# Performance work log

Measured on AMD Instinct MI355X. Metric: run time of the kernel, lower is better.

## Reference

```python
import jax, jax.numpy as jnp
import numpy as np

S = 2048      # sequence length
E = 2048      # n_embd
H = 16        # n_head
D = E // H    # head_dim = 128
EPS = 1e-5


def _layer_norm(x, w):
    # eqx.nn.LayerNorm, use_bias=False: (x - mean) / sqrt(var + eps) * w
    mu = jnp.mean(x, axis=-1, keepdims=True)
    var = jnp.mean(jnp.square(x - mu), axis=-1, keepdims=True)
    return (x - mu) * jax.lax.rsqrt(var + EPS) * w


def setup_inputs() -> dict:
    key = jax.random.key(0)
    ks = jax.random.split(key, 7)
    x = jax.random.normal(ks[0], (S, E), dtype=jnp.float32)
    # equinox Linear weights are (out_features, in_features); y = W @ x
    w_attn = jax.random.normal(ks[1], (3 * E, E), dtype=jnp.float32) * 0.02
    w_proj_attn = jax.random.normal(ks[2], (E, E), dtype=jnp.float32) * 0.02
    w_fc = jax.random.normal(ks[3], (4 * E, E), dtype=jnp.float32) * 0.02
    w_proj_ffn = jax.random.normal(ks[4], (E, 4 * E), dtype=jnp.float32) * 0.02
    ln1_w = jnp.ones((E,), dtype=jnp.float32)
    ln2_w = jnp.ones((E,), dtype=jnp.float32)
    return {"x": x, "ln1_w": ln1_w, "ln2_w": ln2_w, "w_attn": w_attn,
            "w_proj_attn": w_proj_attn, "w_fc": w_fc, "w_proj_ffn": w_proj_ffn}


def reference(x, ln1_w, ln2_w, w_attn, w_proj_attn, w_fc, w_proj_ffn):
    # --- LN1 + fused QKV projection ---
    h = _layer_norm(x, ln1_w)                       # [S, E]
    qkv = h @ w_attn.T                              # [S, 3E]
    q, k, v = jnp.split(qkv, 3, axis=-1)
    q = q.reshape(S, H, D)
    k = k.reshape(S, H, D)
    v = v.reshape(S, H, D)
    # --- naive causal attention with materialized [H, S, T] scores ---
    scale = 1.0 / jnp.sqrt(jnp.float32(D))
    causal_bias = (jnp.arange(S)[:, None] < jnp.arange(S)[None, :]) * (-10000.0)
    scores = jnp.einsum('shd,thd->hst', q, k) * scale + causal_bias  # [H,S,T]
    probs = jax.nn.softmax(scores, axis=-1)
    attn = jnp.einsum('hst,thd->shd', probs, v).reshape(S, E)
    x = x + attn @ w_proj_attn.T
    # --- LN2 + GELU MLP ---
    h2 = _layer_norm(x, ln2_w)                      # [S, E]
    f = jax.nn.gelu(h2 @ w_fc.T) @ w_proj_ffn.T    # [S,4E] -> [S,E]
    return x + f
```

## Files before the change

kernel.cpp:

```cpp
#include <hip/hip_runtime.h>
#include <hip/hip_bf16.h>

#define S_LEN 2048
#define EMB   2048
#define NH    16
#define HD    128

typedef __bf16 bf16x8 __attribute__((ext_vector_type(8)));
typedef __bf16 bf16x4 __attribute__((ext_vector_type(4)));
typedef float  f32x4  __attribute__((ext_vector_type(4)));
typedef short  s16x4  __attribute__((ext_vector_type(4)));

__device__ __forceinline__ void async_copy16(void* lds, const void* g) {
  __builtin_amdgcn_global_load_lds((__attribute__((address_space(1))) void*)(void*)g,
                                   (__attribute__((address_space(3))) void*)lds, 16, 0, 0);
}

__device__ __forceinline__ unsigned lds_addr(const void* p) {
  return (unsigned)(uintptr_t)(const __attribute__((address_space(3))) char*)p;
}

__device__ __forceinline__ s16x4 tr16(unsigned addr) {
  s16x4 d;
  asm volatile("ds_read_b64_tr_b16 %0, %1" : "=v"(d) : "v"(addr));
  return d;
}

__device__ __forceinline__ float gelu_tanh(float x) {
  float x3 = x * x * x;
  float t  = 0.7978845608028654f * (x + 0.044715f * x3);
  float th = 1.0f - 2.0f / (__expf(2.0f * t) + 1.0f);
  return 0.5f * x * (1.0f + th);
}

__global__ __launch_bounds__(256) void cast_kernel(const float* __restrict__ in,
                                                   __bf16* __restrict__ out, int n) {
  int i = (blockIdx.x * 256 + threadIdx.x) * 4;
  if (i >= n) return;
  float4 v = *(const float4*)(in + i);
  bf16x4 o;
  o[0] = (__bf16)v.x; o[1] = (__bf16)v.y; o[2] = (__bf16)v.z; o[3] = (__bf16)v.w;
  *(bf16x4*)(out + i) = o;
}

__global__ __launch_bounds__(256) void ln_kernel(const float* __restrict__ x,
                                                 const float* __restrict__ w,
                                                 __bf16* __restrict__ out) {
  int row = blockIdx.x;
  int t = threadIdx.x;
  const float* xr = x + (size_t)row * EMB;
  float4 a = *(const float4*)(xr + t * 8);
  float4 b = *(const float4*)(xr + t * 8 + 4);
  float s  = a.x + a.y + a.z + a.w + b.x + b.y + b.z + b.w;
  float sq = a.x*a.x + a.y*a.y + a.z*a.z + a.w*a.w + b.x*b.x + b.y*b.y + b.z*b.z + b.w*b.w;
  #pragma unroll
  for (int o = 32; o > 0; o >>= 1) { s += __shfl_xor(s, o); sq += __shfl_xor(sq, o); }
  __shared__ float red[8];
  if ((t & 63) == 0) { red[t >> 6] = s; red[(t >> 6) + 4] = sq; }
  __syncthreads();
  s  = red[0] + red[1] + red[2] + red[3];
  sq = red[4] + red[5] + red[6] + red[7];
  float mu  = s * (1.0f / EMB);
  float var = sq * (1.0f / EMB) - mu * mu;
  float rs  = rsqrtf(var + 1e-5f);
  float4 w1 = *(const float4*)(w + t * 8);
  float4 w2 = *(const float4*)(w + t * 8 + 4);
  bf16x8 ov;
  ov[0] = (__bf16)((a.x - mu) * rs * w1.x);
  ov[1] = (__bf16)((a.y - mu) * rs * w1.y);
  ov[2] = (__bf16)((a.z - mu) * rs * w1.z);
  ov[3] = (__bf16)((a.w - mu) * rs * w1.w);
  ov[4] = (__bf16)((b.x - mu) * rs * w2.x);
  ov[5] = (__bf16)((b.y - mu) * rs * w2.y);
  ov[6] = (__bf16)((b.z - mu) * rs * w2.z);
  ov[7] = (__bf16)((b.w - mu) * rs * w2.w);
  *(bf16x8*)(out + (size_t)row * EMB + t * 8) = ov;
}

__global__ __launch_bounds__(256) void ln_fuse_kernel(const float* __restrict__ x,
                                                      const __bf16* __restrict__ part,
                                                      const float* __restrict__ w,
                                                      __bf16* __restrict__ hout,
                                                      float* __restrict__ resout) {
  int row = blockIdx.x;
  int t = threadIdx.x;
  const size_t base = (size_t)row * EMB + t * 8;
  float r[8];
  {
    float4 a = *(const float4*)(x + base);
    float4 b = *(const float4*)(x + base + 4);
    r[0] = a.x; r[1] = a.y; r[2] = a.z; r[3] = a.w;
    r[4] = b.x; r[5] = b.y; r[6] = b.z; r[7] = b.w;
    #pragma unroll
    for (int z = 0; z < 4; z++) {
      bf16x8 p = *(const bf16x8*)(part + (size_t)z * S_LEN * EMB + base);
      #pragma unroll
      for (int k = 0; k < 8; k++) r[k] += (float)p[k];
    }
  }
  float s = 0.f, sq = 0.f;
  #pragma unroll
  for (int k = 0; k < 8; k++) { s += r[k]; sq += r[k] * r[k]; }
  #pragma unroll
  for (int o = 32; o > 0; o >>= 1) { s += __shfl_xor(s, o); sq += __shfl_xor(sq, o); }
  __shared__ float red[8];
  if ((t & 63) == 0) { red[t >> 6] = s; red[(t >> 6) + 4] = sq; }
  __syncthreads();
  s  = red[0] + red[1] + red[2] + red[3];
  sq = red[4] + red[5] + red[6] + red[7];
  float mu  = s * (1.0f / EMB);
  float var = sq * (1.0f / EMB) - mu * mu;
  float rs  = rsqrtf(var + 1e-5f);
  float4 w1 = *(const float4*)(w + t * 8);
  float4 w2 = *(const float4*)(w + t * 8 + 4);
  float wv[8] = {w1.x, w1.y, w1.z, w1.w, w2.x, w2.y, w2.z, w2.w};
  bf16x8 ov;
  #pragma unroll
  for (int k = 0; k < 8; k++) ov[k] = (__bf16)((r[k] - mu) * rs * wv[k]);
  *(bf16x8*)(hout + base) = ov;
  float4 o1 = make_float4(r[0], r[1], r[2], r[3]);
  float4 o2 = make_float4(r[4], r[5], r[6], r[7]);
  *(float4*)(resout + base) = o1;
  *(float4*)(resout + base + 4) = o2;
}

__global__ __launch_bounds__(256) void add4_kernel(float* __restrict__ out,
                                                   const __bf16* __restrict__ part) {
  size_t i = ((size_t)blockIdx.x * 256 + threadIdx.x) * 4;
  float4 o = *(const float4*)(out + i);
  #pragma unroll
  for (int z = 0; z < 4; z++) {
    bf16x4 p = *(const bf16x4*)(part + (size_t)z * S_LEN * EMB + i);
    o.x += (float)p[0]; o.y += (float)p[1]; o.z += (float)p[2]; o.w += (float)p[3];
  }
  *(float4*)(out + i) = o;
}

#define MFMA16(AV, BV, MG)                                                                   \
  _Pragma("unroll")                                                                          \
  for (int m = 0; m < 4; m++)                                                                \
    _Pragma("unroll")                                                                        \
    for (int n = 0; n < 4; n++)                                                              \
      acc[(MG) * 4 + m][n] =                                                                 \
          __builtin_amdgcn_mfma_f32_16x16x32_bf16(AV[m], BV[n], acc[(MG) * 4 + m][n], 0, 0, 0);

#define PHASE_TOP()                                                                          \
  __builtin_amdgcn_s_barrier();                                                              \
  __builtin_amdgcn_s_setprio(1);

#define PHASE_BOT()                                                                          \
  __builtin_amdgcn_s_setprio(0);                                                             \
  __builtin_amdgcn_s_barrier();

template <int EPI>
__global__ __launch_bounds__(512, 2) void gemm256(const __bf16* __restrict__ A,
                                                  const __bf16* __restrict__ B,
                                                  void* __restrict__ Cv,
                                                  int M, int N, int K, int Ksl,
                                                  int NN, int NSPLIT) {
  __shared__ __bf16 As[2 * 2 * 256 * 32];
  __shared__ __bf16 Bs[2 * 2 * 256 * 32];

  const int t = threadIdx.x, w = t >> 6, l = t & 63;
  const int fr = l & 15, g = l >> 4;
  const int wr = w >> 2, wc = w & 3;

  const int nwg = gridDim.x;
  const int wg = (blockIdx.x & 7) * (nwg >> 3) + (blockIdx.x >> 3);
  const int z = wg % NSPLIT;
  const int tile = wg / NSPLIT;
  const int my = tile / NN, nx = tile - my * NN;
  const int m0 = my * 256, n0 = nx * 256;
  const int kb = z * Ksl;
  const int NT = Ksl >> 6;

  const int srow = t >> 2;
  const int schunk = (t & 3) ^ ((t >> 3) & 3);
  const __bf16* Abase = A + (size_t)(m0 + srow) * K + kb + schunk * 8;
  const __bf16* Bbase = B + (size_t)(n0 + srow) * K + kb + schunk * 8;
  const size_t K128 = (size_t)128 * K;
  __bf16* AsT = &As[t * 8];
  __bf16* BsT = &Bs[t * 8];

  auto stage = [&](const __bf16* base, __bf16* dstT, int kt, int kh) {
    const __bf16* src = base + kt * 64 + kh * 32;
    __bf16* dst = dstT + ((kt & 1) * 2 + kh) * 8192;
    async_copy16(dst, src);
    async_copy16(dst + 4096, src + K128);
  };

  const int gran = (g ^ ((fr >> 1) & 3)) << 3;
  auto rdA = [&](bf16x8* dst, int kt, int kh, int mg) {
    const int ub = ((kt & 1) * 2 + kh) * 256;
    #pragma unroll
    for (int m = 0; m < 4; m++) {
      int row = wr * 128 + (mg * 4 + m) * 16 + fr;
      dst[m] = *(const bf16x8*)&As[(ub + row) * 32 + gran];
    }
  };
  auto rdB = [&](bf16x8* dst, int kt, int kh) {
    const int ub = ((kt & 1) * 2 + kh) * 256;
    #pragma unroll
    for (int n = 0; n < 4; n++) {
      int row = wc * 64 + n * 16 + fr;
      dst[n] = *(const bf16x8*)&Bs[(ub + row) * 32 + gran];
    }
  };

  f32x4 acc[8][4] = {};
  bf16x8 av[4], bX[4], bY[4];

  stage(Abase, AsT, 0, 0); stage(Bbase, BsT, 0, 0);
  stage(Abase, AsT, 0, 1); stage(Bbase, BsT, 0, 1);
  if (NT > 1) { stage(Abase, AsT, 1, 0); stage(Bbase, BsT, 1, 0); }
  asm volatile("s_waitcnt vmcnt(4)" ::: "memory");
  __builtin_amdgcn_s_barrier();

  for (int kt = 0; kt < NT; ++kt) {
    const bool s1 = (kt + 1 < NT), s2 = (kt + 2 < NT);
    rdB(bX, kt, 0);
    rdA(av, kt, 0, 0);
    if (s1) stage(Abase, AsT, kt + 1, 1);
    PHASE_TOP();
    MFMA16(av, bX, 0);
    PHASE_BOT();
    rdA(av, kt, 0, 1);
    if (s1) stage(Bbase, BsT, kt + 1, 1);
    PHASE_TOP();
    MFMA16(av, bX, 1);
    __builtin_amdgcn_s_setprio(0);
    if (s1) { asm volatile("s_waitcnt vmcnt(4)" ::: "memory"); }
    else    { asm volatile("s_waitcnt vmcnt(0)" ::: "memory"); }
    __builtin_amdgcn_s_barrier();
    rdB(bY, kt, 1);
    rdA(av, kt, 1, 0);
    if (s2) stage(Abase, AsT, kt + 2, 0);
    PHASE_TOP();
    MFMA16(av, bY, 0);
    PHASE_BOT();
    rdA(av, kt, 1, 1);
    if (s2) stage(Bbase, BsT, kt + 2, 0);
    PHASE_TOP();
    MFMA16(av, bY, 1);
    PHASE_BOT();
  }

  const size_t zoff = (size_t)z * M * N;
  #pragma unroll
  for (int m = 0; m < 8; m++)
    #pragma unroll
    for (int n = 0; n < 4; n++)
      #pragma unroll
      for (int j = 0; j < 4; j++) {
        int orow = m0 + wr * 128 + m * 16 + g * 4 + j;
        int ocol = n0 + wc * 64 + n * 16 + fr;
        size_t idx = (size_t)orow * N + ocol;
        float v = acc[m][n][j];
        if (EPI == 0) {
          ((__bf16*)Cv)[idx] = (__bf16)v;
        } else if (EPI == 2) {
          ((__bf16*)Cv)[idx] = (__bf16)gelu_tanh(v);
        } else {
          ((__bf16*)Cv)[zoff + idx] = (__bf16)v;
        }
      }
}

__global__ __launch_bounds__(512, 2) void attn_kernel(const __bf16* __restrict__ qkv,
                                                      __bf16* __restrict__ out) {
  __shared__ __bf16 Kt[2][64 * 128];
  __shared__ __bf16 Vt[2][64 * 128];
  __shared__ __bf16 Pb[8][16 * 64];

  const int bid = blockIdx.x;
  const int h = bid & 15;
  const int pi = bid >> 4;
  const int qbA = pi, qbB = 31 - pi;

  const int t = threadIdx.x, w = t >> 6, l = t & 63;
  const int g = l >> 4, fr = l & 15;
  const int fkb = g * 8;
  const int myqb = (w < 4) ? qbA : qbB;
  const int q0 = myqb * 64 + (w & 3) * 16;
  const float scale = 0.08838834764831845f;

  const int kchunk = fr ^ ((w * 4 + g) & 7);
  const int vkey = (l >> 1) & 3;
  const int vd0  = (l >> 3) * 16 + (l & 1) * 8;

  const size_t row3E = (size_t)(3 * EMB);
  const __bf16* Kg = qkv + EMB + h * HD;
  const __bf16* Vg = qkv + 2 * EMB + h * HD;

  bf16x8 qf[4];
  #pragma unroll
  for (int kc = 0; kc < 4; kc++)
    qf[kc] = *(const bf16x8*)&qkv[(size_t)(q0 + fr) * row3E + h * HD + kc * 32 + fkb];

  f32x4 o[8] = {};
  float mrun[4] = {-1e30f, -1e30f, -1e30f, -1e30f};
  float lsum[4] = {0.f, 0.f, 0.f, 0.f};

  const unsigned vtrb[2] = { lds_addr(&Vt[0][0]) + g * 2048 + fr * 8,
                             lds_addr(&Vt[1][0]) + g * 2048 + fr * 8 };

  auto stage = [&](int buf, int it) {
    const int t0 = it * 64;
    #pragma unroll
    for (int r = 0; r < 2; r++) {
      async_copy16(&Kt[buf][(r * 8 + w) * 512],
                   Kg + (size_t)(t0 + (r * 8 + w) * 4 + g) * row3E + kchunk * 8);
      async_copy16(&Vt[buf][(r * 8 + w) * 512],
                   Vg + (size_t)(t0 + (r * 8 + w) * 4 + vkey) * row3E + vd0);
    }
  };

  const int nt = qbB + 1;
  stage(0, 0);
  int cur = 0;

  for (int it = 0; it < nt; it++) {
    __syncthreads();
    if (it + 1 < nt) stage(cur ^ 1, it + 1);

    if (it <= myqb) {
      const int t0 = it * 64;
      f32x4 s[4] = {};
      __builtin_amdgcn_s_setprio(1);
      #pragma unroll
      for (int n = 0; n < 4; n++)
        #pragma unroll
        for (int kc = 0; kc < 4; kc++) {
          bf16x8 kf = *(const bf16x8*)&Kt[cur][(n * 16 + fr) * 128 +
                                              (((kc * 4 + g) ^ (fr & 7)) << 3)];
          s[n] = __builtin_amdgcn_mfma_f32_16x16x32_bf16(qf[kc], kf, s[n], 0, 0, 0);
        }
      __builtin_amdgcn_s_setprio(0);
      #pragma unroll
      for (int n = 0; n < 4; n++)
        #pragma unroll
        for (int j = 0; j < 4; j++) {
          int tcol = t0 + n * 16 + fr;
          int qrow = q0 + g * 4 + j;
          float v = s[n][j] * scale;
          s[n][j] = (tcol > qrow) ? -1e30f : v;
        }
      float pm[4];
      #pragma unroll
      for (int j = 0; j < 4; j++) {
        pm[j] = fmaxf(fmaxf(s[0][j], s[1][j]), fmaxf(s[2][j], s[3][j]));
        #pragma unroll
        for (int off = 1; off < 16; off <<= 1) pm[j] = fmaxf(pm[j], __shfl_xor(pm[j], off));
      }
      float factor[4];
      #pragma unroll
      for (int j = 0; j < 4; j++) {
        float mn = fmaxf(mrun[j], pm[j]);
        factor[j] = __expf(mrun[j] - mn);
        mrun[j] = mn;
      }
      float rs[4] = {0.f, 0.f, 0.f, 0.f};
      #pragma unroll
      for (int n = 0; n < 4; n++)
        #pragma unroll
        for (int j = 0; j < 4; j++) {
          float p = __expf(s[n][j] - mrun[j]);
          s[n][j] = p;
          rs[j] += p;
        }
      #pragma unroll
      for (int j = 0; j < 4; j++) {
        #pragma unroll
        for (int off = 1; off < 16; off <<= 1) rs[j] += __shfl_xor(rs[j], off);
        lsum[j] = lsum[j] * factor[j] + rs[j];
      }
      #pragma unroll
      for (int b = 0; b < 8; b++)
        #pragma unroll
        for (int j = 0; j < 4; j++) o[b][j] *= factor[j];

      #pragma unroll
      for (int n = 0; n < 4; n++)
        #pragma unroll
        for (int j = 0; j < 4; j++) {
          int q   = g * 4 + j;
          int key = n * 16 + fr;
          int cs  = (key >> 3) ^ (q & 7);
          Pb[w][q * 64 + cs * 8 + (key & 7)] = (__bf16)s[n][j];
        }

      bf16x8 pf[2];
      #pragma unroll
      for (int kc = 0; kc < 2; kc++)
        pf[kc] = *(const bf16x8*)&Pb[w][fr * 64 + (((kc * 4 + g) ^ (fr & 7)) << 3)];

      const unsigned vtr = vtrb[cur];
      __builtin_amdgcn_s_setprio(1);
      #pragma unroll
      for (int b = 0; b < 8; b++) {
        s16x4 t00 = tr16(vtr + b * 128);
        s16x4 t01 = tr16(vtr + b * 128 + 1024);
        s16x4 t10 = tr16(vtr + b * 128 + 8192);
        s16x4 t11 = tr16(vtr + b * 128 + 8192 + 1024);
        asm volatile("s_waitcnt lgkmcnt(0)");
        __builtin_amdgcn_sched_barrier(0);
        union { s16x4 hh[2]; bf16x8 v; } u0, u1;
        u0.hh[0] = t00; u0.hh[1] = t01;
        u1.hh[0] = t10; u1.hh[1] = t11;
        o[b] = __builtin_amdgcn_mfma_f32_16x16x32_bf16(pf[0], u0.v, o[b], 0, 0, 0);
        o[b] = __builtin_amdgcn_mfma_f32_16x16x32_bf16(pf[1], u1.v, o[b], 0, 0, 0);
      }
      __builtin_amdgcn_s_setprio(0);
    }
    cur ^= 1;
  }

  float rcp[4];
  #pragma unroll
  for (int j = 0; j < 4; j++) rcp[j] = 1.0f / lsum[j];
  #pragma unroll
  for (int b = 0; b < 8; b++)
    #pragma unroll
    for (int j = 0; j < 4; j++) {
      int qrow = q0 + g * 4 + j;
      out[(size_t)qrow * EMB + h * HD + b * 16 + fr] = (__bf16)(o[b][j] * rcp[j]);
    }
}

extern "C" void kernel_launch(void* const* d_in, const int* in_sizes, int n_in,
                              void* d_out, int out_size, void* d_ws, size_t ws_size,
                              hipStream_t stream) {
  const float* x     = (const float*)d_in[0];
  const float* ln1w  = (const float*)d_in[1];
  const float* ln2w  = (const float*)d_in[2];
  const float* wattn = (const float*)d_in[3];
  const float* wproja= (const float*)d_in[4];
  const float* wfc   = (const float*)d_in[5];
  const float* wprojf= (const float*)d_in[6];
  float* out = (float*)d_out;
  char* ws = (char*)d_ws;

  __bf16* wattn_b  = (__bf16*)(ws);
  __bf16* wproja_b = (__bf16*)(ws + 25165824);
  __bf16* wfc_b    = (__bf16*)(ws + 33554432);
  __bf16* wprojf_b = (__bf16*)(ws + 67108864);
  __bf16* h_b      = (__bf16*)(ws + 100663296);
  __bf16* qkv_b    = (__bf16*)(ws + 109051904);
  __bf16* attn_b   = (__bf16*)(ws + 134217728);
  __bf16* f1_b     = (__bf16*)(ws + 142606336);
  __bf16* p1_part  = f1_b;
  __bf16* p2_part  = qkv_b;

  cast_kernel<<<12288, 256, 0, stream>>>(wattn,  wattn_b,  12582912);
  cast_kernel<<<4096,  256, 0, stream>>>(wproja, wproja_b, 4194304);
  cast_kernel<<<16384, 256, 0, stream>>>(wfc,    wfc_b,    16777216);
  cast_kernel<<<16384, 256, 0, stream>>>(wprojf, wprojf_b, 16777216);

  ln_kernel<<<S_LEN, 256, 0, stream>>>(x, ln1w, h_b);
  gemm256<0><<<192, 512, 0, stream>>>(h_b, wattn_b, qkv_b, S_LEN, 3 * EMB, EMB, EMB, 24, 1);
  attn_kernel<<<dim3(256), 512, 0, stream>>>(qkv_b, attn_b);
  gemm256<5><<<256, 512, 0, stream>>>(attn_b, wproja_b, p1_part, S_LEN, EMB, EMB, EMB / 4, 8, 4);
  ln_fuse_kernel<<<S_LEN, 256, 0, stream>>>(x, p1_part, ln2w, h_b, out);
  gemm256<2><<<256, 512, 0, stream>>>(h_b, wfc_b, f1_b, S_LEN, 4 * EMB, EMB, EMB, 32, 1);
  gemm256<5><<<256, 512, 0, stream>>>(f1_b, wprojf_b, p2_part, S_LEN, EMB, 4 * EMB, 2048, 8, 4);
  add4_kernel<<<4096, 256, 0, stream>>>(out, p2_part);
}
```

Measured before the change: 403.7 us.

## Replace 256x256 GEMM with 128x256 tile, 3-stage K32 pipeline

Replaces the 256x256 GEMM tile, which double-buffered K=64 in two halves, with a 128x256 tile that uses a triple-buffered K=32 LDS pipeline and one barrier per iteration. The launch grids double and launch bounds raise occupancy to 4 blocks per CU, aiming to fill all CUs better and cut per-wave accumulator registers. The trade-off is lower arithmetic intensity per tile, more global traffic for B, and more barriers per unit of K work.

Result: slower. 418.1 us (+3.5%).

```diff
diff --git a/kernel.cpp b/kernel.cpp
--- a/kernel.cpp
+++ b/kernel.cpp
@@ -136,30 +136,14 @@
   *(float4*)(out + i) = o;
 }
 
-#define MFMA16(AV, BV, MG)                                                                   \
-  _Pragma("unroll")                                                                          \
-  for (int m = 0; m < 4; m++)                                                                \
-    _Pragma("unroll")                                                                        \
-    for (int n = 0; n < 4; n++)                                                              \
-      acc[(MG) * 4 + m][n] =                                                                 \
-          __builtin_amdgcn_mfma_f32_16x16x32_bf16(AV[m], BV[n], acc[(MG) * 4 + m][n], 0, 0, 0);
-
-#define PHASE_TOP()                                                                          \
-  __builtin_amdgcn_s_barrier();                                                              \
-  __builtin_amdgcn_s_setprio(1);
-
-#define PHASE_BOT()                                                                          \
-  __builtin_amdgcn_s_setprio(0);                                                             \
-  __builtin_amdgcn_s_barrier();
-
 template <int EPI>
-__global__ __launch_bounds__(512, 2) void gemm256(const __bf16* __restrict__ A,
+__global__ __launch_bounds__(512, 4) void gemm128(const __bf16* __restrict__ A,
                                                   const __bf16* __restrict__ B,
                                                   void* __restrict__ Cv,
                                                   int M, int N, int K, int Ksl,
                                                   int NN, int NSPLIT) {
-  __shared__ __bf16 As[2 * 2 * 256 * 32];
-  __shared__ __bf16 Bs[2 * 2 * 256 * 32];
+  __shared__ __bf16 As[3][128 * 32];
+  __shared__ __bf16 Bs[3][256 * 32];
 
   const int t = threadIdx.x, w = t >> 6, l = t & 63;
   const int fr = l & 15, g = l >> 4;
@@ -170,89 +154,66 @@
   const int z = wg % NSPLIT;
   const int tile = wg / NSPLIT;
   const int my = tile / NN, nx = tile - my * NN;
-  const int m0 = my * 256, n0 = nx * 256;
+  const int m0 = my * 128, n0 = nx * 256;
   const int kb = z * Ksl;
-  const int NT = Ksl >> 6;
+  const int NT = Ksl >> 5;
 
   const int srow = t >> 2;
   const int schunk = (t & 3) ^ ((t >> 3) & 3);
   const __bf16* Abase = A + (size_t)(m0 + srow) * K + kb + schunk * 8;
   const __bf16* Bbase = B + (size_t)(n0 + srow) * K + kb + schunk * 8;
   const size_t K128 = (size_t)128 * K;
-  __bf16* AsT = &As[t * 8];
-  __bf16* BsT = &Bs[t * 8];
-
-  auto stage = [&](const __bf16* base, __bf16* dstT, int kt, int kh) {
-    const __bf16* src = base + kt * 64 + kh * 32;
-    __bf16* dst = dstT + ((kt & 1) * 2 + kh) * 8192;
-    async_copy16(dst, src);
-    async_copy16(dst + 4096, src + K128);
+
+  auto stage = [&](int kt, int slot) {
+    const __bf16* sa = Abase + kt * 32;
+    const __bf16* sb = Bbase + kt * 32;
+    async_copy16(&As[slot][t * 8], sa);
+    async_copy16(&Bs[slot][t * 8], sb);
+    async_copy16(&Bs[slot][t * 8 + 4096], sb + K128);
   };
 
   const int gran = (g ^ ((fr >> 1) & 3)) << 3;
-  auto rdA = [&](bf16x8* dst, int kt, int kh, int mg) {
-    const int ub = ((kt & 1) * 2 + kh) * 256;
-    #pragma unroll
-    for (int m = 0; m < 4; m++) {
-      int row = wr * 128 + (mg * 4 + m) * 16 + fr;
-      dst[m] = *(const bf16x8*)&As[(ub + row) * 32 + gran];
+
+  f32x4 acc[4][4] = {};
+
+  stage(0, 0);
+  stage(1, 1);
+  asm volatile("s_waitcnt vmcnt(3)" ::: "memory");
+  __builtin_amdgcn_s_barrier();
+
+  int sc = 0, s1 = 1, s2 = 2;
+  for (int kt = 0; kt < NT; ++kt) {
+    bf16x8 a[4], b[4];
+    #pragma unroll
+    for (int m = 0; m < 4; m++)
+      a[m] = *(const bf16x8*)&As[sc][(wr * 64 + m * 16 + fr) * 32 + gran];
+    #pragma unroll
+    for (int n = 0; n < 4; n++)
+      b[n] = *(const bf16x8*)&Bs[sc][(wc * 64 + n * 16 + fr) * 32 + gran];
+    if (kt + 2 < NT) stage(kt + 2, s2);
+    __builtin_amdgcn_s_setprio(1);
+    #pragma unroll
+    for (int m = 0; m < 4; m++)
+      #pragma unroll
+      for (int n = 0; n < 4; n++)
+        acc[m][n] = __builtin_amdgcn_mfma_f32_16x16x32_bf16(a[m], b[n], acc[m][n], 0, 0, 0);
+    __builtin_amdgcn_s_setprio(0);
+    if (kt + 1 < NT) {
+      if (kt + 2 < NT) { asm volatile("s_waitcnt vmcnt(3)" ::: "memory"); }
+      else             { asm volatile("s_waitcnt vmcnt(0)" ::: "memory"); }
     }
-  };
-  auto rdB = [&](bf16x8* dst, int kt, int kh) {
-    const int ub = ((kt & 1) * 2 + kh) * 256;
-    #pragma unroll
-    for (int n = 0; n < 4; n++) {
-      int row = wc * 64 + n * 16 + fr;
-      dst[n] = *(const bf16x8*)&Bs[(ub + row) * 32 + gran];
-    }
-  };
-
-  f32x4 acc[8][4] = {};
-  bf16x8 av[4], bX[4], bY[4];
-
-  stage(Abase, AsT, 0, 0); stage(Bbase, BsT, 0, 0);
-  stage(Abase, AsT, 0, 1); stage(Bbase, BsT, 0, 1);
-  if (NT > 1) { stage(Abase, AsT, 1, 0); stage(Bbase, BsT, 1, 0); }
-  asm volatile("s_waitcnt vmcnt(4)" ::: "memory");
-  __builtin_amdgcn_s_barrier();
-
-  for (int kt = 0; kt < NT; ++kt) {
-    const bool s1 = (kt + 1 < NT), s2 = (kt + 2 < NT);
-    rdB(bX, kt, 0);
-    rdA(av, kt, 0, 0);
-    if (s1) stage(Abase, AsT, kt + 1, 1);
-    PHASE_TOP();
-    MFMA16(av, bX, 0);
-    PHASE_BOT();
-    rdA(av, kt, 0, 1);
-    if (s1) stage(Bbase, BsT, kt + 1, 1);
-    PHASE_TOP();
-    MFMA16(av, bX, 1);
-    __builtin_amdgcn_s_setprio(0);
-    if (s1) { asm volatile("s_waitcnt vmcnt(4)" ::: "memory"); }
-    else    { asm volatile("s_waitcnt vmcnt(0)" ::: "memory"); }
     __builtin_amdgcn_s_barrier();
-    rdB(bY, kt, 1);
-    rdA(av, kt, 1, 0);
-    if (s2) stage(Abase, AsT, kt + 2, 0);
-    PHASE_TOP();
-    MFMA16(av, bY, 0);
-    PHASE_BOT();
-    rdA(av, kt, 1, 1);
-    if (s2) stage(Bbase, BsT, kt + 2, 0);
-    PHASE_TOP();
-    MFMA16(av, bY, 1);
-    PHASE_BOT();
+    int tmp = sc; sc = s1; s1 = s2; s2 = tmp;
   }
 
   const size_t zoff = (size_t)z * M * N;
   #pragma unroll
-  for (int m = 0; m < 8; m++)
+  for (int m = 0; m < 4; m++)
     #pragma unroll
     for (int n = 0; n < 4; n++)
       #pragma unroll
       for (int j = 0; j < 4; j++) {
-        int orow = m0 + wr * 128 + m * 16 + g * 4 + j;
+        int orow = m0 + wr * 64 + m * 16 + g * 4 + j;
         int ocol = n0 + wc * 64 + n * 16 + fr;
         size_t idx = (size_t)orow * N + ocol;
         float v = acc[m][n][j];
@@ -457,11 +418,11 @@
   cast_kernel<<<16384, 256, 0, stream>>>(wprojf, wprojf_b, 16777216);
 
   ln_kernel<<<S_LEN, 256, 0, stream>>>(x, ln1w, h_b);
-  gemm256<0><<<192, 512, 0, stream>>>(h_b, wattn_b, qkv_b, S_LEN, 3 * EMB, EMB, EMB, 24, 1);
+  gemm128<0><<<384, 512, 0, stream>>>(h_b, wattn_b, qkv_b, S_LEN, 3 * EMB, EMB, EMB, 24, 1);
   attn_kernel<<<dim3(256), 512, 0, stream>>>(qkv_b, attn_b);
-  gemm256<5><<<256, 512, 0, stream>>>(attn_b, wproja_b, p1_part, S_LEN, EMB, EMB, EMB / 4, 8, 4);
+  gemm128<5><<<512, 512, 0, stream>>>(attn_b, wproja_b, p1_part, S_LEN, EMB, EMB, EMB / 4, 8, 4);
   ln_fuse_kernel<<<S_LEN, 256, 0, stream>>>(x, p1_part, ln2w, h_b, out);
-  gemm256<2><<<256, 512, 0, stream>>>(h_b, wfc_b, f1_b, S_LEN, 4 * EMB, EMB, EMB, 32, 1);
-  gemm256<5><<<256, 512, 0, stream>>>(f1_b, wprojf_b, p2_part, S_LEN, EMB, 4 * EMB, 2048, 8, 4);
+  gemm128<2><<<512, 512, 0, stream>>>(h_b, wfc_b, f1_b, S_LEN, 4 * EMB, EMB, EMB, 32, 1);
+  gemm128<5><<<512, 512, 0, stream>>>(f1_b, wprojf_b, p2_part, S_LEN, EMB, 4 * EMB, 2048, 8, 4);
   add4_kernel<<<4096, 256, 0, stream>>>(out, p2_part);
 }
```

## Merge weight casts into one launch and use 128x256-tile GEMM for FFN

Applied to the files above, without the earlier changes.

Replaces the four per-weight cast launches with a single kernel that picks source and destination by index range, removing three launches. Adds a gemm128 kernel with 128x256 tiles and a triple-buffered LDS pipeline that allows four workgroups per CU, and uses it for both FFN GEMMs with 512 workgroups instead of 256. The smaller tiles give more parallelism and better CU fill on the FFN matmuls, at the cost of less operand reuse per tile and more global traffic.

Result: slower. 413.7 us (+2.5%).

```diff
diff --git a/kernel.cpp b/kernel.cpp
--- a/kernel.cpp
+++ b/kernel.cpp
@@ -33,14 +33,24 @@
   return 0.5f * x * (1.0f + th);
 }
 
-__global__ __launch_bounds__(256) void cast_kernel(const float* __restrict__ in,
-                                                   __bf16* __restrict__ out, int n) {
-  int i = (blockIdx.x * 256 + threadIdx.x) * 4;
-  if (i >= n) return;
-  float4 v = *(const float4*)(in + i);
+__global__ __launch_bounds__(256) void cast_all(const float* __restrict__ s0,
+                                                const float* __restrict__ s1,
+                                                const float* __restrict__ s2,
+                                                const float* __restrict__ s3,
+                                                __bf16* __restrict__ d0,
+                                                __bf16* __restrict__ d1,
+                                                __bf16* __restrict__ d2,
+                                                __bf16* __restrict__ d3) {
+  size_t i = ((size_t)blockIdx.x * 256 + threadIdx.x) * 4;
+  const float* s; __bf16* d; size_t off;
+  if (i < 12582912ull)       { s = s0; d = d0; off = i; }
+  else if (i < 16777216ull)  { s = s1; d = d1; off = i - 12582912ull; }
+  else if (i < 33554432ull)  { s = s2; d = d2; off = i - 16777216ull; }
+  else                       { s = s3; d = d3; off = i - 33554432ull; }
+  float4 v = *(const float4*)(s + off);
   bf16x4 o;
   o[0] = (__bf16)v.x; o[1] = (__bf16)v.y; o[2] = (__bf16)v.z; o[3] = (__bf16)v.w;
-  *(bf16x4*)(out + i) = o;
+  *(bf16x4*)(d + off) = o;
 }
 
 __global__ __launch_bounds__(256) void ln_kernel(const float* __restrict__ x,
@@ -266,6 +276,97 @@
       }
 }
 
+template <int EPI>
+__global__ __launch_bounds__(512, 4) void gemm128(const __bf16* __restrict__ A,
+                                                  const __bf16* __restrict__ B,
+                                                  void* __restrict__ Cv,
+                                                  int M, int N, int K, int Ksl,
+                                                  int NN, int NSPLIT) {
+  __shared__ __bf16 As[3][128 * 32];
+  __shared__ __bf16 Bs[3][256 * 32];
+
+  const int t = threadIdx.x, w = t >> 6, l = t & 63;
+  const int fr = l & 15, g = l >> 4;
+  const int wr = w >> 2, wc = w & 3;
+
+  const int nwg = gridDim.x;
+  const int wg = (blockIdx.x & 7) * (nwg >> 3) + (blockIdx.x >> 3);
+  const int z = wg % NSPLIT;
+  const int tile = wg / NSPLIT;
+  const int my = tile / NN, nx = tile - my * NN;
+  const int m0 = my * 128, n0 = nx * 256;
+  const int kb = z * Ksl;
+  const int NT = Ksl >> 5;
+
+  const int srow = t >> 2;
+  const int schunk = (t & 3) ^ ((t >> 3) & 3);
+  const __bf16* Abase = A + (size_t)(m0 + srow) * K + kb + schunk * 8;
+  const __bf16* Bbase = B + (size_t)(n0 + srow) * K + kb + schunk * 8;
+  const size_t K128 = (size_t)128 * K;
+
+  auto stage = [&](int kt, int slot) {
+    const __bf16* sa = Abase + kt * 32;
+    const __bf16* sb = Bbase + kt * 32;
+    async_copy16(&As[slot][t * 8], sa);
+    async_copy16(&Bs[slot][t * 8], sb);
+    async_copy16(&Bs[slot][t * 8 + 4096], sb + K128);
+  };
+
+  const int gran = (g ^ ((fr >> 1) & 3)) << 3;
+
+  f32x4 acc[4][4] = {};
+
+  stage(0, 0);
+  stage(1, 1);
+  asm volatile("s_waitcnt vmcnt(3)" ::: "memory");
+  __builtin_amdgcn_s_barrier();
+
+  int sc = 0, s1 = 1, s2 = 2;
+  for (int kt = 0; kt < NT; ++kt) {
+    bf16x8 a[4], b[4];
+    #pragma unroll
+    for (int m = 0; m < 4; m++)
+      a[m] = *(const bf16x8*)&As[sc][(wr * 64 + m * 16 + fr) * 32 + gran];
+    #pragma unroll
+    for (int n = 0; n < 4; n++)
+      b[n] = *(const bf16x8*)&Bs[sc][(wc * 64 + n * 16 + fr) * 32 + gran];
+    if (kt + 2 < NT) stage(kt + 2, s2);
+    __builtin_amdgcn_s_setprio(1);
+    #pragma unroll
+    for (int m = 0; m < 4; m++)
+      #pragma unroll
+      for (int n = 0; n < 4; n++)
+        acc[m][n] = __builtin_amdgcn_mfma_f32_16x16x32_bf16(a[m], b[n], acc[m][n], 0, 0, 0);
+    __builtin_amdgcn_s_setprio(0);
+    if (kt + 1 < NT) {
+      if (kt + 2 < NT) { asm volatile("s_waitcnt vmcnt(3)" ::: "memory"); }
+      else             { asm volatile("s_waitcnt vmcnt(0)" ::: "memory"); }
+    }
+    __builtin_amdgcn_s_barrier();
+    int tmp = sc; sc = s1; s1 = s2; s2 = tmp;
+  }
+
+  const size_t zoff = (size_t)z * M * N;
+  #pragma unroll
+  for (int m = 0; m < 4; m++)
+    #pragma unroll
+    for (int n = 0; n < 4; n++)
+      #pragma unroll
+      for (int j = 0; j < 4; j++) {
+        int orow = m0 + wr * 64 + m * 16 + g * 4 + j;
+        int ocol = n0 + wc * 64 + n * 16 + fr;
+        size_t idx = (size_t)orow * N + ocol;
+        float v = acc[m][n][j];
+        if (EPI == 0) {
+          ((__bf16*)Cv)[idx] = (__bf16)v;
+        } else if (EPI == 2) {
+          ((__bf16*)Cv)[idx] = (__bf16)gelu_tanh(v);
+        } else {
+          ((__bf16*)Cv)[zoff + idx] = (__bf16)v;
+        }
+      }
+}
+
 __global__ __launch_bounds__(512, 2) void attn_kernel(const __bf16* __restrict__ qkv,
                                                       __bf16* __restrict__ out) {
   __shared__ __bf16 Kt[2][64 * 128];
@@ -451,17 +552,15 @@
   __bf16* p1_part  = f1_b;
   __bf16* p2_part  = qkv_b;
 
-  cast_kernel<<<12288, 256, 0, stream>>>(wattn,  wattn_b,  12582912);
-  cast_kernel<<<4096,  256, 0, stream>>>(wproja, wproja_b, 4194304);
-  cast_kernel<<<16384, 256, 0, stream>>>(wfc,    wfc_b,    16777216);
-  cast_kernel<<<16384, 256, 0, stream>>>(wprojf, wprojf_b, 16777216);
+  cast_all<<<49152, 256, 0, stream>>>(wattn, wproja, wfc, wprojf,
+                                      wattn_b, wproja_b, wfc_b, wprojf_b);
 
   ln_kernel<<<S_LEN, 256, 0, stream>>>(x, ln1w, h_b);
   gemm256<0><<<192, 512, 0, stream>>>(h_b, wattn_b, qkv_b, S_LEN, 3 * EMB, EMB, EMB, 24, 1);
   attn_kernel<<<dim3(256), 512, 0, stream>>>(qkv_b, attn_b);
   gemm256<5><<<256, 512, 0, stream>>>(attn_b, wproja_b, p1_part, S_LEN, EMB, EMB, EMB / 4, 8, 4);
   ln_fuse_kernel<<<S_LEN, 256, 0, stream>>>(x, p1_part, ln2w, h_b, out);
-  gemm256<2><<<256, 512, 0, stream>>>(h_b, wfc_b, f1_b, S_LEN, 4 * EMB, EMB, EMB, 32, 1);
-  gemm256<5><<<256, 512, 0, stream>>>(f1_b, wprojf_b, p2_part, S_LEN, EMB, 4 * EMB, 2048, 8, 4);
+  gemm128<2><<<512, 512, 0, stream>>>(h_b, wfc_b, f1_b, S_LEN, 4 * EMB, EMB, EMB, 32, 1);
+  gemm128<5><<<512, 512, 0, stream>>>(f1_b, wprojf_b, p2_part, S_LEN, EMB, 4 * EMB, 2048, 8, 4);
   add4_kernel<<<4096, 256, 0, stream>>>(out, p2_part);
 }
```
